# Kernel optimization log

Measured on AMD Instinct MI355X. Metric: run time of the kernel, lower is better.

The kernel has to match this reference:

```python
import jax, jax.numpy as jnp
import numpy as np

REF_CHANNEL = 0
DIAG_EPS = 1e-7   # diag_loading coefficient
TIK_EPS = 1e-8    # additive eps in diagonal loading / trace denominator
MASK_EPS = 1e-15  # PSD mask-normalization eps


def _psd(spec, mask):
    # spec: (b, c, f, t) complex; mask: (b, f, t) real
    # PSD module: normalize mask over time, weight outer products, sum over t.
    m = mask / (mask.sum(axis=-1, keepdims=True) + MASK_EPS)
    return jnp.einsum('bcft,beft,bft->bfce', spec, spec.conj(), m.astype(spec.dtype))


def setup_inputs() -> dict:
    key = jax.random.key(0)
    k1, k2, k3, k4 = jax.random.split(key, 4)
    B, C, F, T = 4, 6, 257, 2000
    return {
        'spec_real': jax.random.normal(k1, (B, C, F, T), dtype=jnp.float32),
        'spec_imag': jax.random.normal(k2, (B, C, F, T), dtype=jnp.float32),
        'mask_s': jax.random.uniform(k3, (B, F, T), dtype=jnp.float32),
        'mask_n': jax.random.uniform(k4, (B, F, T), dtype=jnp.float32),
    }


def reference(spec_real, spec_imag, mask_s, mask_n):
    spec = spec_real + 1j * spec_imag                     # (b, c, f, t) complex64
    C = spec.shape[1]

    psd_s = _psd(spec, mask_s)                            # (b, f, c, c)
    psd_n = _psd(spec, mask_n)                            # (b, f, c, c)

    # Diagonal loading (Tikhonov regularization) of the noise PSD.
    tr_n = jnp.einsum('bfcc->bf', psd_n).real
    epsilon = jax.lax.stop_gradient(tr_n * DIAG_EPS + TIK_EPS)   # torch uses no_grad here
    psd_n = psd_n + epsilon[..., None, None] * jnp.eye(C, dtype=spec.dtype)

    # ref_channel solution: w = (psd_n^-1 psd_s) / trace(psd_n^-1 psd_s) @ u
    numerator = jnp.linalg.solve(psd_n, psd_s)            # (b, f, c, c)
    tr = jnp.einsum('bfcc->bf', numerator)
    ws = numerator / (tr[..., None, None] + TIK_EPS)
    w = ws[..., :, REF_CHANNEL]                           # one-hot u selects column -> (b, f, c)

    # enhanced = w^H Y
    enh = jnp.einsum('bfc,bcft->bft', w.conj(), spec)     # (b, f, t) complex
    return jnp.stack([enh.real, enh.imag], axis=-1)       # (b, f, t, 2) float32
```

## Files before the change

kernel.cpp:

```cpp
#include <hip/hip_runtime.h>

#define NB 4
#define NC 6
#define NF 257
#define NT 2000
#define NG (NB * NF)
#define NPAIR 15
#define NACC 74
#define NACCS 37
#define PSTR 40
#define NCHUNK 4
#define TCH (NT / NCHUNK)
#define NP2 (TCH / 2)
#define BLK 256
#define CS  (NF * NT)
#define CS2 (CS / 2)

typedef float nfloat4 __attribute__((ext_vector_type(4)));

template<int CTRL>
__device__ __forceinline__ float dpp_add(float v) {
    int s = __builtin_amdgcn_update_dpp(0, __builtin_bit_cast(int, v), CTRL, 0xF, 0xF, true);
    return v + __builtin_bit_cast(float, s);
}

__global__ __launch_bounds__(BLK) void psd_kernel(
    const float* __restrict__ sr, const float* __restrict__ si,
    const float* __restrict__ ms, const float* __restrict__ mn,
    float* __restrict__ wsp)
{
    constexpr int PC[NPAIR] = {0,0,0,0,0,1,1,1,1,2,2,2,3,3,4};
    constexpr int PE[NPAIR] = {1,2,3,4,5,2,3,4,5,3,4,5,4,5,5};

    const int bx     = blockIdx.x;
    const int g      = bx >> 3;
    const int rem    = bx & 7;
    const int chunk  = rem >> 1;
    const int parity = rem & 1;
    const int b  = g / NF;
    const int f  = g - b * NF;
    const int tb = chunk * TCH;
    const int sbase = b * NC * CS + f * NT + tb;
    const int mbase = g * NT + tb;

    const float2* s2r = (const float2*)(sr + sbase);
    const float2* s2i = (const float2*)(si + sbase);
    const float2* m2  = (const float2*)((parity ? mn : ms) + mbase);

    float acc[NACCS];
    #pragma unroll
    for (int i = 0; i < NACCS; i++) acc[i] = 0.f;

    const bool act = threadIdx.x < NP2;
    const int  p   = act ? threadIdx.x : 0;
    {
        float wm[2], rr[NC][2], ii[NC][2];
        {
            const float2 t0 = m2[p];
            wm[0] = t0.x; wm[1] = t0.y;
        }
        #pragma unroll
        for (int c = 0; c < NC; c++) {
            const float2 tr = s2r[c * CS2 + p];
            rr[c][0] = tr.x; rr[c][1] = tr.y;
            const float2 ti = s2i[c * CS2 + p];
            ii[c][0] = ti.x; ii[c][1] = ti.y;
        }
        if (!act) { wm[0] = wm[1] = 0.f; }
        #pragma unroll
        for (int k = 0; k < 2; k++) acc[36] += wm[k];
        #pragma unroll
        for (int c = 0; c < NC; c++) {
            #pragma unroll
            for (int k = 0; k < 2; k++) {
                const float d = rr[c][k] * rr[c][k] + ii[c][k] * ii[c][k];
                acc[c] += d * wm[k];
            }
        }
        #pragma unroll
        for (int q = 0; q < NPAIR; q++) {
            const int c = PC[q], e = PE[q];
            #pragma unroll
            for (int k = 0; k < 2; k++) {
                const float cr = rr[c][k] * rr[e][k] + ii[c][k] * ii[e][k];
                const float ci = ii[c][k] * rr[e][k] - rr[c][k] * ii[e][k];
                acc[6 + 2 * q]     += cr * wm[k];
                acc[6 + 2 * q + 1] += ci * wm[k];
            }
        }
    }

    #pragma unroll
    for (int i = 0; i < NACCS; i++) {
        float v = acc[i];
        v = dpp_add<0x118>(v);
        v = dpp_add<0x114>(v);
        v = dpp_add<0x112>(v);
        acc[i] = v;
    }

    __shared__ float red[32][NACCS];
    const int lane16 = threadIdx.x & 15;
    const int ridx   = ((threadIdx.x >> 4) << 1) | (lane16 & 1);
    if (lane16 >= 14) {
        #pragma unroll
        for (int i = 0; i < NACCS; i++) red[ridx][i] = acc[i];
    }
    __syncthreads();

    if (threadIdx.x < NACCS) {
        float s = 0.f;
        #pragma unroll
        for (int r = 0; r < 32; r++) s += red[r][threadIdx.x];
        wsp[bx * PSTR + threadIdx.x] = s;
    }
}

__global__ __launch_bounds__(64, 1) void solve_kernel(
    const float* __restrict__ wsp, float* __restrict__ wsw)
{
    const int gid = blockIdx.x * 64 + threadIdx.x;
    if (gid >= NG) return;

    constexpr int PC[NPAIR] = {0,0,0,0,0,1,1,1,1,2,2,2,3,3,4};
    constexpr int PE[NPAIR] = {1,2,3,4,5,2,3,4,5,3,4,5,4,5,5};
    constexpr int QIDX[NC][NC] = {
        {-1, 0, 1, 2, 3, 4},
        {-1,-1, 5, 6, 7, 8},
        {-1,-1,-1, 9,10,11},
        {-1,-1,-1,-1,12,13},
        {-1,-1,-1,-1,-1,14},
        {-1,-1,-1,-1,-1,-1}};

    const float* p0 = wsp + (8 * gid) * PSTR;
    float fs[NACCS], fn[NACCS];
    #pragma unroll
    for (int i = 0; i < NACCS; i++) {
        fs[i] = (p0[0 * PSTR + i] + p0[2 * PSTR + i]) + (p0[4 * PSTR + i] + p0[6 * PSTR + i]);
        fn[i] = (p0[1 * PSTR + i] + p0[3 * PSTR + i]) + (p0[5 * PSTR + i] + p0[7 * PSTR + i]);
    }
    float fin[NACC];
    #pragma unroll
    for (int c = 0; c < NC; c++) { fin[c] = fs[c]; fin[6 + c] = fn[c]; }
    #pragma unroll
    for (int q = 0; q < NPAIR; q++) {
        fin[12 + 4 * q + 0] = fs[6 + 2 * q];
        fin[12 + 4 * q + 1] = fs[6 + 2 * q + 1];
        fin[12 + 4 * q + 2] = fn[6 + 2 * q];
        fin[12 + 4 * q + 3] = fn[6 + 2 * q + 1];
    }
    fin[72] = fs[36];
    fin[73] = fn[36];

    const float invS = 1.f / (fin[72] + 1e-15f);
    const float invN = 1.f / (fin[73] + 1e-15f);

    float Ar[NC][NC], Ai[NC][NC];
    #pragma unroll
    for (int c = 0; c < NC; c++) { Ar[c][c] = fin[6 + c] * invN; Ai[c][c] = 0.f; }
    #pragma unroll
    for (int q = 0; q < NPAIR; q++) {
        const int c = PC[q], e = PE[q];
        const float nre = fin[12 + 4 * q + 2] * invN;
        const float nim = fin[12 + 4 * q + 3] * invN;
        Ar[c][e] = nre;  Ai[c][e] = nim;
        Ar[e][c] = nre;  Ai[e][c] = -nim;
    }
    {
        float trn = 0.f;
        #pragma unroll
        for (int c = 0; c < NC; c++) trn += Ar[c][c];
        const float eps = trn * 1e-7f + 1e-8f;
        #pragma unroll
        for (int c = 0; c < NC; c++) Ar[c][c] += eps;
    }

    #pragma unroll
    for (int k = 0; k < NC; k++) {
        const float dr = Ar[k][k], di = Ai[k][k];
        const float idn = 1.f / (dr * dr + di * di);
        const float pr = dr * idn, pi = -di * idn;
        #pragma unroll
        for (int i = k + 1; i < NC; i++) {
            const float lr = Ar[i][k] * pr - Ai[i][k] * pi;
            const float li = Ar[i][k] * pi + Ai[i][k] * pr;
            Ar[i][k] = lr; Ai[i][k] = li;
            #pragma unroll
            for (int j = k + 1; j < NC; j++) {
                Ar[i][j] -= lr * Ar[k][j] - li * Ai[k][j];
                Ai[i][j] -= lr * Ai[k][j] + li * Ar[k][j];
            }
        }
    }

    float trr = 1e-8f, tri = 0.f;
    float w0r[NC], w0i[NC];
    #pragma unroll
    for (int j = 0; j < NC; j++) {
        float xr[NC], xi[NC];
        #pragma unroll
        for (int i = 0; i < NC; i++) {
            if (i == j)      { xr[i] = fin[j] * invS;                      xi[i] = 0.f; }
            else if (i < j)  { const int q = QIDX[i][j];
                               xr[i] = fin[12 + 4 * q] * invS;  xi[i] =  fin[13 + 4 * q] * invS; }
            else             { const int q = QIDX[j][i];
                               xr[i] = fin[12 + 4 * q] * invS;  xi[i] = -fin[13 + 4 * q] * invS; }
        }
        #pragma unroll
        for (int i = 1; i < NC; i++) {
            #pragma unroll
            for (int k = 0; k < NC - 1; k++) if (k < i) {
                xr[i] -= Ar[i][k] * xr[k] - Ai[i][k] * xi[k];
                xi[i] -= Ar[i][k] * xi[k] + Ai[i][k] * xr[k];
            }
        }
        #pragma unroll
        for (int i = NC - 1; i >= 0; i--) {
            #pragma unroll
            for (int k = 0; k < NC; k++) if (k > i) {
                xr[i] -= Ar[i][k] * xr[k] - Ai[i][k] * xi[k];
                xi[i] -= Ar[i][k] * xi[k] + Ai[i][k] * xr[k];
            }
            const float dr = Ar[i][i], di = Ai[i][i];
            const float idn = 1.f / (dr * dr + di * di);
            const float pr = dr * idn, pi = -di * idn;
            const float tr0 = xr[i] * pr - xi[i] * pi;
            xi[i] = xr[i] * pi + xi[i] * pr;
            xr[i] = tr0;
        }
        trr += xr[j]; tri += xi[j];
        if (j == 0) {
            #pragma unroll
            for (int i = 0; i < NC; i++) { w0r[i] = xr[i]; w0i[i] = xi[i]; }
        }
    }

    const float idn = 1.f / (trr * trr + tri * tri);
    #pragma unroll
    for (int c = 0; c < NC; c++) {
        const float wre = (w0r[c] * trr + w0i[c] * tri) * idn;
        const float wim = (w0i[c] * trr - w0r[c] * tri) * idn;
        wsw[gid * 12 + c]     = wre;
        wsw[gid * 12 + 6 + c] = -wim;
    }
}

#define ACHUNK 2
#define ATCH (NT / ACHUNK)
#define ANP4 (ATCH / 4)
#define CS4 (CS / 4)

__global__ __launch_bounds__(BLK) void apply_kernel(
    const float* __restrict__ sr, const float* __restrict__ si,
    const float* __restrict__ wsw, float* __restrict__ out)
{
    const int bx = blockIdx.x;
    const int g  = bx >> 1;
    const int b  = g / NF;
    const int f  = g - b * NF;
    const int tb = (bx & 1) * ATCH;
    const int sbase = b * NC * CS + f * NT + tb;

    const nfloat4* s4r = (const nfloat4*)(sr + sbase);
    const nfloat4* s4i = (const nfloat4*)(si + sbase);

    float wr[NC], wi[NC];
    #pragma unroll
    for (int c = 0; c < NC; c++) {
        wr[c] = wsw[g * 12 + c];
        wi[c] = wsw[g * 12 + 6 + c];
    }

    nfloat4* o4 = (nfloat4*)(out + 2 * (g * NT + tb));

    const int p = threadIdx.x;
    if (p < ANP4) {
        float rr[NC][4], ii[NC][4];
        #pragma unroll
        for (int c = 0; c < NC; c++) {
            const nfloat4 tr = s4r[c * CS4 + p];
            rr[c][0] = tr.x; rr[c][1] = tr.y; rr[c][2] = tr.z; rr[c][3] = tr.w;
            const nfloat4 ti = s4i[c * CS4 + p];
            ii[c][0] = ti.x; ii[c][1] = ti.y; ii[c][2] = ti.z; ii[c][3] = ti.w;
        }
        float er[4], ei[4];
        #pragma unroll
        for (int k = 0; k < 4; k++) {
            float a = 0.f, bb = 0.f;
            #pragma unroll
            for (int c = 0; c < NC; c++) {
                a  += wr[c] * rr[c][k] - wi[c] * ii[c][k];
                bb += wr[c] * ii[c][k] + wi[c] * rr[c][k];
            }
            er[k] = a; ei[k] = bb;
        }
        nfloat4 o0 = {er[0], ei[0], er[1], ei[1]};
        nfloat4 o1 = {er[2], ei[2], er[3], ei[3]};
        __builtin_nontemporal_store(o0, &o4[2 * p]);
        __builtin_nontemporal_store(o1, &o4[2 * p + 1]);
    }
}

extern "C" void kernel_launch(void* const* d_in, const int* in_sizes, int n_in,
                              void* d_out, int out_size, void* d_ws, size_t ws_size,
                              hipStream_t stream) {
    const float* sr = (const float*)d_in[0];
    const float* si = (const float*)d_in[1];
    const float* ms = (const float*)d_in[2];
    const float* mn = (const float*)d_in[3];
    float* out = (float*)d_out;

    float* wsp = (float*)d_ws;
    float* wsw = wsp + NG * 8 * PSTR;

    psd_kernel<<<NG * NCHUNK * 2, BLK, 0, stream>>>(sr, si, ms, mn, wsp);
    solve_kernel<<<(NG + 63) / 64, 64, 0, stream>>>(wsp, wsw);
    apply_kernel<<<NG * ACHUNK, BLK, 0, stream>>>(sr, si, wsw, out);
}
```

Before: 174.4 us.

## Merge speech and noise PSD blocks to load each spectrum tile once

The PSD kernel previously launched separate blocks per mask (parity), so each spectrum chunk was read from global memory twice. Each block now loads both masks, runs the speech and noise accumulation passes on the same registers, and writes the full 74-entry interleaved layout. The solve kernel's read pattern changes to match. This halves spectrum traffic and block count, at the cost of more registers and work per block, which may reduce occupancy.

```diff
diff --git a/kernel.cpp b/kernel.cpp
--- a/kernel.cpp
+++ b/kernel.cpp
@@ -8,7 +8,6 @@
 #define NPAIR 15
 #define NACC 74
 #define NACCS 37
-#define PSTR 40
 #define NCHUNK 4
 #define TCH (NT / NCHUNK)
 #define NP2 (TCH / 2)
@@ -24,69 +23,37 @@
     return v + __builtin_bit_cast(float, s);
 }
 
-__global__ __launch_bounds__(BLK) void psd_kernel(
-    const float* __restrict__ sr, const float* __restrict__ si,
-    const float* __restrict__ ms, const float* __restrict__ mn,
-    float* __restrict__ wsp)
+template<int PAR>
+__device__ __forceinline__ void psd_pass(
+    const float wm[2], const float rr[NC][2], const float ii[NC][2],
+    float (*red)[NACC], int tid)
 {
     constexpr int PC[NPAIR] = {0,0,0,0,0,1,1,1,1,2,2,2,3,3,4};
     constexpr int PE[NPAIR] = {1,2,3,4,5,2,3,4,5,3,4,5,4,5,5};
 
-    const int bx     = blockIdx.x;
-    const int g      = bx >> 3;
-    const int rem    = bx & 7;
-    const int chunk  = rem >> 1;
-    const int parity = rem & 1;
-    const int b  = g / NF;
-    const int f  = g - b * NF;
-    const int tb = chunk * TCH;
-    const int sbase = b * NC * CS + f * NT + tb;
-    const int mbase = g * NT + tb;
-
-    const float2* s2r = (const float2*)(sr + sbase);
-    const float2* s2i = (const float2*)(si + sbase);
-    const float2* m2  = (const float2*)((parity ? mn : ms) + mbase);
-
     float acc[NACCS];
     #pragma unroll
     for (int i = 0; i < NACCS; i++) acc[i] = 0.f;
 
-    const bool act = threadIdx.x < NP2;
-    const int  p   = act ? threadIdx.x : 0;
-    {
-        float wm[2], rr[NC][2], ii[NC][2];
-        {
-            const float2 t0 = m2[p];
-            wm[0] = t0.x; wm[1] = t0.y;
-        }
-        #pragma unroll
-        for (int c = 0; c < NC; c++) {
-            const float2 tr = s2r[c * CS2 + p];
-            rr[c][0] = tr.x; rr[c][1] = tr.y;
-            const float2 ti = s2i[c * CS2 + p];
-            ii[c][0] = ti.x; ii[c][1] = ti.y;
-        }
-        if (!act) { wm[0] = wm[1] = 0.f; }
-        #pragma unroll
-        for (int k = 0; k < 2; k++) acc[36] += wm[k];
-        #pragma unroll
-        for (int c = 0; c < NC; c++) {
-            #pragma unroll
-            for (int k = 0; k < 2; k++) {
-                const float d = rr[c][k] * rr[c][k] + ii[c][k] * ii[c][k];
-                acc[c] += d * wm[k];
-            }
-        }
-        #pragma unroll
-        for (int q = 0; q < NPAIR; q++) {
-            const int c = PC[q], e = PE[q];
-            #pragma unroll
-            for (int k = 0; k < 2; k++) {
-                const float cr = rr[c][k] * rr[e][k] + ii[c][k] * ii[e][k];
-                const float ci = ii[c][k] * rr[e][k] - rr[c][k] * ii[e][k];
-                acc[6 + 2 * q]     += cr * wm[k];
-                acc[6 + 2 * q + 1] += ci * wm[k];
-            }
+    #pragma unroll
+    for (int k = 0; k < 2; k++) acc[36] += wm[k];
+    #pragma unroll
+    for (int c = 0; c < NC; c++) {
+        #pragma unroll
+        for (int k = 0; k < 2; k++) {
+            const float d = rr[c][k] * rr[c][k] + ii[c][k] * ii[c][k];
+            acc[c] += d * wm[k];
+        }
+    }
+    #pragma unroll
+    for (int q = 0; q < NPAIR; q++) {
+        const int c = PC[q], e = PE[q];
+        #pragma unroll
+        for (int k = 0; k < 2; k++) {
+            const float cr = rr[c][k] * rr[e][k] + ii[c][k] * ii[e][k];
+            const float ci = ii[c][k] * rr[e][k] - rr[c][k] * ii[e][k];
+            acc[6 + 2 * q]     += cr * wm[k];
+            acc[6 + 2 * q + 1] += ci * wm[k];
         }
     }
 
@@ -99,20 +66,71 @@
         acc[i] = v;
     }
 
-    __shared__ float red[32][NACCS];
-    const int lane16 = threadIdx.x & 15;
-    const int ridx   = ((threadIdx.x >> 4) << 1) | (lane16 & 1);
+    const int lane16 = tid & 15;
+    const int ridx   = ((tid >> 4) << 1) | (lane16 & 1);
     if (lane16 >= 14) {
         #pragma unroll
-        for (int i = 0; i < NACCS; i++) red[ridx][i] = acc[i];
-    }
+        for (int c = 0; c < NC; c++) red[ridx][PAR ? 6 + c : c] = acc[c];
+        #pragma unroll
+        for (int q = 0; q < NPAIR; q++) {
+            red[ridx][12 + 4 * q + 2 * PAR]     = acc[6 + 2 * q];
+            red[ridx][12 + 4 * q + 2 * PAR + 1] = acc[6 + 2 * q + 1];
+        }
+        red[ridx][72 + PAR] = acc[36];
+    }
+}
+
+__global__ __launch_bounds__(BLK) void psd_kernel(
+    const float* __restrict__ sr, const float* __restrict__ si,
+    const float* __restrict__ ms, const float* __restrict__ mn,
+    float* __restrict__ wsp)
+{
+    const int bx = blockIdx.x;
+    const int g  = bx >> 2;
+    const int b  = g / NF;
+    const int f  = g - b * NF;
+    const int tb = (bx & 3) * TCH;
+    const int sbase = b * NC * CS + f * NT + tb;
+    const int mbase = g * NT + tb;
+    const int tid = threadIdx.x;
+
+    const float2* s2r = (const float2*)(sr + sbase);
+    const float2* s2i = (const float2*)(si + sbase);
+    const float2* m2s = (const float2*)(ms + mbase);
+    const float2* m2n = (const float2*)(mn + mbase);
+
+    __shared__ float red[32][NACC];
+
+    const bool act = tid < NP2;
+    const int  p   = act ? tid : 0;
+
+    float wms[2], wmn[2], rr[NC][2], ii[NC][2];
+    {
+        const float2 t0 = m2s[p];
+        wms[0] = t0.x; wms[1] = t0.y;
+        const float2 t1 = m2n[p];
+        wmn[0] = t1.x; wmn[1] = t1.y;
+    }
+    #pragma unroll
+    for (int c = 0; c < NC; c++) {
+        const float2 tr = s2r[c * CS2 + p];
+        rr[c][0] = tr.x; rr[c][1] = tr.y;
+        const float2 ti = s2i[c * CS2 + p];
+        ii[c][0] = ti.x; ii[c][1] = ti.y;
+    }
+    if (!act) { wms[0] = wms[1] = wmn[0] = wmn[1] = 0.f; }
+
+    psd_pass<0>(wms, rr, ii, red, tid);
+    __builtin_amdgcn_sched_barrier(0);
+    psd_pass<1>(wmn, rr, ii, red, tid);
+
     __syncthreads();
 
-    if (threadIdx.x < NACCS) {
+    if (tid < NACC) {
         float s = 0.f;
         #pragma unroll
-        for (int r = 0; r < 32; r++) s += red[r][threadIdx.x];
-        wsp[bx * PSTR + threadIdx.x] = s;
+        for (int r = 0; r < 32; r++) s += red[r][tid];
+        wsp[bx * NACC + tid] = s;
     }
 }
 
@@ -132,25 +150,11 @@
         {-1,-1,-1,-1,-1,14},
         {-1,-1,-1,-1,-1,-1}};
 
-    const float* p0 = wsp + (8 * gid) * PSTR;
-    float fs[NACCS], fn[NACCS];
-    #pragma unroll
-    for (int i = 0; i < NACCS; i++) {
-        fs[i] = (p0[0 * PSTR + i] + p0[2 * PSTR + i]) + (p0[4 * PSTR + i] + p0[6 * PSTR + i]);
-        fn[i] = (p0[1 * PSTR + i] + p0[3 * PSTR + i]) + (p0[5 * PSTR + i] + p0[7 * PSTR + i]);
-    }
+    const float* p0 = wsp + (NCHUNK * gid) * NACC;
     float fin[NACC];
     #pragma unroll
-    for (int c = 0; c < NC; c++) { fin[c] = fs[c]; fin[6 + c] = fn[c]; }
-    #pragma unroll
-    for (int q = 0; q < NPAIR; q++) {
-        fin[12 + 4 * q + 0] = fs[6 + 2 * q];
-        fin[12 + 4 * q + 1] = fs[6 + 2 * q + 1];
-        fin[12 + 4 * q + 2] = fn[6 + 2 * q];
-        fin[12 + 4 * q + 3] = fn[6 + 2 * q + 1];
-    }
-    fin[72] = fs[36];
-    fin[73] = fn[36];
+    for (int i = 0; i < NACC; i++)
+        fin[i] = (p0[i] + p0[NACC + i]) + (p0[2 * NACC + i] + p0[3 * NACC + i]);
 
     const float invS = 1.f / (fin[72] + 1e-15f);
     const float invN = 1.f / (fin[73] + 1e-15f);
@@ -311,9 +315,9 @@
     float* out = (float*)d_out;
 
     float* wsp = (float*)d_ws;
-    float* wsw = wsp + NG * 8 * PSTR;
-
-    psd_kernel<<<NG * NCHUNK * 2, BLK, 0, stream>>>(sr, si, ms, mn, wsp);
+    float* wsw = wsp + NG * NCHUNK * NACC;
+
+    psd_kernel<<<NG * NCHUNK, BLK, 0, stream>>>(sr, si, ms, mn, wsp);
     solve_kernel<<<(NG + 63) / 64, 64, 0, stream>>>(wsp, wsw);
     apply_kernel<<<NG * ACHUNK, BLK, 0, stream>>>(sr, si, wsw, out);
 }
```

After: 162.3 us. -7.0%, faster.
